# Kernel optimization log

Measured on AMD Instinct MI355X. Metric: run time of the kernel, lower is better.

## Reference

```python
import jax, jax.numpy as jnp
import numpy as np

D_MODEL = 1024
NUM_HEADS = 16
D_HEAD = D_MODEL // NUM_HEADS
PATCH = 128


def setup_inputs() -> dict:
    key = jax.random.key(0)
    ks = jax.random.split(key, 10)
    B, T = 4, 8192
    x = jax.random.normal(ks[0], (B, T, D_MODEL), dtype=jnp.float32)
    coords = jax.random.uniform(ks[1], (B, T, 2), dtype=jnp.float32)
    s = 1.0 / np.sqrt(D_MODEL)
    Wq = jax.random.normal(ks[2], (D_MODEL, D_MODEL), dtype=jnp.float32) * s
    Wk = jax.random.normal(ks[3], (D_MODEL, D_MODEL), dtype=jnp.float32) * s
    Wv = jax.random.normal(ks[4], (D_MODEL, D_MODEL), dtype=jnp.float32) * s
    Wo = jax.random.normal(ks[5], (D_MODEL, D_MODEL), dtype=jnp.float32) * s
    bq = jnp.zeros((D_MODEL,), jnp.float32)
    bk = jnp.zeros((D_MODEL,), jnp.float32)
    bv = jnp.zeros((D_MODEL,), jnp.float32)
    bo = jnp.zeros((D_MODEL,), jnp.float32)
    return {"x": x, "coords": coords, "Wq": Wq, "bq": bq, "Wk": Wk, "bk": bk,
            "Wv": Wv, "bv": bv, "Wo": Wo, "bo": bo}


def _patched_attn(x, Wq, bq, Wk, bk, Wv, bv, Wo, bo):
    B, T, D = x.shape
    P = PATCH
    pad_len = (P - T % P) % P
    if pad_len > 0:
        x = jnp.pad(x, ((0, 0), (0, pad_len), (0, 0)))
    Tp = T + pad_len
    n = Tp // P
    xp = x.reshape(B * n, P, D)  # [N, P, D], independent patches
    def heads(y):  # [N, P, D] -> [N, H, P, dh]
        return y.reshape(B * n, P, NUM_HEADS, D_HEAD).transpose(0, 2, 1, 3)
    q = heads(xp @ Wq + bq)
    k = heads(xp @ Wk + bk)
    v = heads(xp @ Wv + bv)
    scores = jnp.einsum('bhtd,bhTd->bhtT', q, k) / jnp.sqrt(jnp.asarray(D_HEAD, x.dtype))
    w = jax.nn.softmax(scores, axis=-1)
    out = jnp.einsum('bhtT,bhTd->bhtd', w, v)
    out = out.transpose(0, 2, 1, 3).reshape(B * n, P, D)
    out = out @ Wo + bo
    out = out.reshape(B, Tp, D)
    if pad_len > 0:
        out = out[:, :T, :]
    return out


def reference(x, coords, Wq, bq, Wk, bk, Wv, bv, Wo, bo):
    # coords participates only in padding/reshape, not in the math
    return _patched_attn(x, Wq, bq, Wk, bk, Wv, bv, Wo, bo)
```

## Files before the change

### kernel.cpp

```cpp
#include <hip/hip_runtime.h>
#include <hip/hip_bf16.h>


#define DEV static __device__ __forceinline__

typedef __attribute__((ext_vector_type(8))) short short8;
typedef __attribute__((ext_vector_type(4))) float f32x4;

DEV unsigned short f2b(float f) {
  unsigned u = __builtin_bit_cast(unsigned, f);
  u += 0x7fffu + ((u >> 16) & 1u);
  return (unsigned short)(u >> 16);
}

DEV void load_lds16(const void* g, void* l) {
  __builtin_amdgcn_global_load_lds(
      (const __attribute__((address_space(1))) void*)g,
      (__attribute__((address_space(3))) void*)l, 16, 0, 0);
}

#define MFMA_BF16(a, b, c) __builtin_amdgcn_mfma_f32_16x16x32_bf16((a), (b), (c), 0, 0, 0)
#define SB0() __builtin_amdgcn_sched_barrier(0)
#define BAR() __builtin_amdgcn_s_barrier()


__global__ void cvt_x_k(const float* __restrict__ x, unsigned short* __restrict__ xb, int n4) {
  int i = blockIdx.x * blockDim.x + threadIdx.x;
  int stride = gridDim.x * blockDim.x;
  for (; i < n4; i += stride) {
    float4 v = ((const float4*)x)[i];
    ushort4 o;
    o.x = f2b(v.x); o.y = f2b(v.y); o.z = f2b(v.z); o.w = f2b(v.w);
    ((ushort4*)xb)[i] = o;
  }
}

__global__ void twk4(const float* __restrict__ W0, const float* __restrict__ W1,
                     const float* __restrict__ W2, const float* __restrict__ W3,
                     unsigned short* __restrict__ Dqkv, unsigned short* __restrict__ Dot) {
  __shared__ unsigned short tile[64][65];
  const int w = blockIdx.x >> 8;
  const int t = blockIdx.x & 255;
  const float* W = (w == 0) ? W0 : (w == 1) ? W1 : (w == 2) ? W2 : W3;
  unsigned short* Wt = (w == 3) ? Dot : Dqkv + (size_t)w * 1024 * 1024;
  int k0 = (t >> 4) << 6;
  int n0 = (t & 15) << 6;
  int tx = threadIdx.x & 63;
  int ty = threadIdx.x >> 6;
#pragma unroll
  for (int i = 0; i < 16; ++i) {
    int r = (i << 2) + ty;
    tile[r][tx] = f2b(W[(size_t)(k0 + r) * 1024 + n0 + tx]);
  }
  __syncthreads();
#pragma unroll
  for (int i = 0; i < 16; ++i) {
    int n = (i << 2) + ty;
    Wt[(size_t)(n0 + n) * 1024 + k0 + tx] = tile[tx][n];
  }
}

__global__ void fuse_bias_k(const float* __restrict__ bq, const float* __restrict__ bk,
                            const float* __restrict__ bv, float* __restrict__ bqkv) {
  int i = blockIdx.x * 256 + threadIdx.x;
  if (i < 1024) bqkv[i] = bq[i];
  else if (i < 2048) bqkv[i] = bk[i - 1024];
  else if (i < 3072) bqkv[i] = bv[i - 2048];
}


template <bool OUT_F32>
__global__ __launch_bounds__(512, 2)
void gemm256(const unsigned short* __restrict__ A,
             const unsigned short* __restrict__ Bt,
             const float* __restrict__ bias,
             void* __restrict__ Cv, int M, int N, int K) {
  __shared__ __align__(16) unsigned short sh[65536];

  int nwg = gridDim.x, bid = blockIdx.x, wg = bid;
  if ((nwg & 7) == 0) {
    int cpx = nwg >> 3;
    wg = (bid & 7) * cpx + (bid >> 3);
  }
  const int nbn = N >> 8;
  const int bm = wg / nbn, bn = wg - bm * nbn;

  const int tid = threadIdx.x, lane = tid & 63, w = tid >> 6;
  const int wm = w >> 2, wn = w & 3;
  const int fr = lane & 15, g = lane >> 4;

  const int lr = lane >> 3;
  const int lb = ((lane & 7) << 4) ^ (lr << 4);
  const unsigned short* gsrc = (w < 4)
      ? A  + (size_t)(bm * 256 + w * 64 + lr) * K + (lb >> 1)
      : Bt + (size_t)(bn * 256 + (w - 4) * 64 + lr) * K + (lb >> 1);
  const int ldsw = w * 8192;

  const int koff0 = (g * 16) ^ ((fr & 7) << 4);
  const int koff1 = koff0 ^ 64;

  f32x4 acc[8][4] = {};
  const int NT = K >> 6;

  short8 a0[4][2], a1[4][2], b0[2][2], b1[2][2];

  {
    char* l0 = (char*)sh + ldsw;
    char* l1 = (char*)sh + 65536 + ldsw;
#pragma unroll
    for (int c = 0; c < 8; ++c)
      load_lds16(gsrc + (size_t)c * 8 * K, l0 + c * 1024);
#pragma unroll
    for (int c = 0; c < 8; ++c)
      load_lds16(gsrc + 64 + (size_t)c * 8 * K, l1 + c * 1024);
    asm volatile("s_waitcnt vmcnt(8)" ::: "memory");
    BAR();
    const char* ap = (const char*)sh + (wm * 128 + fr) * 128;
    const char* bp = (const char*)sh + 32768 + (wn * 64 + fr) * 128;
#pragma unroll
    for (int ii = 0; ii < 4; ++ii) {
      a0[ii][0] = *(const short8*)(ap + ii * 2048 + koff0);
      a0[ii][1] = *(const short8*)(ap + ii * 2048 + koff1);
    }
#pragma unroll
    for (int jj = 0; jj < 2; ++jj) {
      b0[jj][0] = *(const short8*)(bp + jj * 2048 + koff0);
      b0[jj][1] = *(const short8*)(bp + jj * 2048 + koff1);
    }
  }

  for (int t = 0; t < NT; ++t) {
    const char* bufc = (const char*)sh + (t & 1) * 65536;
    const char* bufn = (const char*)sh + ((t + 1) & 1) * 65536;
    const char* apc = bufc + (wm * 128 + fr) * 128;
    const char* bpc = bufc + 32768 + (wn * 64 + fr) * 128;

#pragma unroll
    for (int jj = 0; jj < 2; ++jj) {
      b1[jj][0] = *(const short8*)(bpc + 32 * 128 + jj * 2048 + koff0);
      b1[jj][1] = *(const short8*)(bpc + 32 * 128 + jj * 2048 + koff1);
    }
    BAR();
    asm volatile("s_waitcnt lgkmcnt(4)" ::: "memory");
    SB0();
    __builtin_amdgcn_s_setprio(1);
#pragma unroll
    for (int s = 0; s < 2; ++s)
#pragma unroll
      for (int ii = 0; ii < 4; ++ii)
#pragma unroll
        for (int jj = 0; jj < 2; ++jj)
          acc[ii][jj] = MFMA_BF16(a0[ii][s], b0[jj][s], acc[ii][jj]);
    __builtin_amdgcn_s_setprio(0);
    BAR();

#pragma unroll
    for (int ii = 0; ii < 4; ++ii) {
      a1[ii][0] = *(const short8*)(apc + 64 * 128 + ii * 2048 + koff0);
      a1[ii][1] = *(const short8*)(apc + 64 * 128 + ii * 2048 + koff1);
    }
    BAR();
    asm volatile("s_waitcnt lgkmcnt(8)" ::: "memory");
    SB0();
    __builtin_amdgcn_s_setprio(1);
#pragma unroll
    for (int s = 0; s < 2; ++s)
#pragma unroll
      for (int ii = 0; ii < 4; ++ii)
#pragma unroll
        for (int jj = 0; jj < 2; ++jj)
          acc[ii][2 + jj] = MFMA_BF16(a0[ii][s], b1[jj][s], acc[ii][2 + jj]);
    __builtin_amdgcn_s_setprio(0);
    SB0();
    asm volatile("s_waitcnt lgkmcnt(0)" ::: "memory");
    BAR();

    if (t + 2 < NT) {
      const unsigned short* sN = gsrc + (size_t)(t + 2) * 64;
      char* lN = (char*)sh + (t & 1) * 65536 + ldsw;
#pragma unroll
      for (int c = 0; c < 8; ++c)
        load_lds16(sN + (size_t)c * 8 * K, lN + c * 1024);
    }
    __builtin_amdgcn_s_setprio(1);
#pragma unroll
    for (int s = 0; s < 2; ++s)
#pragma unroll
      for (int ii = 0; ii < 4; ++ii)
#pragma unroll
        for (int jj = 0; jj < 2; ++jj)
          acc[4 + ii][2 + jj] = MFMA_BF16(a1[ii][s], b1[jj][s], acc[4 + ii][2 + jj]);
    __builtin_amdgcn_s_setprio(0);
    if (t + 2 < NT) {
      asm volatile("s_waitcnt vmcnt(8)" ::: "memory");
    } else {
      asm volatile("s_waitcnt vmcnt(0)" ::: "memory");
    }
    BAR();

    __builtin_amdgcn_s_setprio(1);
#pragma unroll
    for (int s = 0; s < 2; ++s)
#pragma unroll
      for (int ii = 0; ii < 4; ++ii)
#pragma unroll
        for (int jj = 0; jj < 2; ++jj)
          acc[4 + ii][jj] = MFMA_BF16(a1[ii][s], b0[jj][s], acc[4 + ii][jj]);
    __builtin_amdgcn_s_setprio(0);
    SB0();
    if (t + 1 < NT) {
      const char* apn = bufn + (wm * 128 + fr) * 128;
      const char* bpn = bufn + 32768 + (wn * 64 + fr) * 128;
#pragma unroll
      for (int ii = 0; ii < 4; ++ii) {
        a0[ii][0] = *(const short8*)(apn + ii * 2048 + koff0);
        a0[ii][1] = *(const short8*)(apn + ii * 2048 + koff1);
      }
#pragma unroll
      for (int jj = 0; jj < 2; ++jj) {
        b0[jj][0] = *(const short8*)(bpn + jj * 2048 + koff0);
        b0[jj][1] = *(const short8*)(bpn + jj * 2048 + koff1);
      }
    }
    SB0();
    BAR();
  }

  const int grow0 = bm * 256 + wm * 128 + g * 4;
  const int gcol0 = bn * 256 + wn * 64 + fr;
  float bv_[4];
#pragma unroll
  for (int j = 0; j < 4; ++j) bv_[j] = bias[gcol0 + j * 16];
#pragma unroll
  for (int i = 0; i < 8; ++i) {
    const int gr = grow0 + i * 16;
#pragma unroll
    for (int r = 0; r < 4; ++r) {
#pragma unroll
      for (int j = 0; j < 4; ++j) {
        float v = acc[i][j][r] + bv_[j];
        if (OUT_F32) ((float*)Cv)[(size_t)(gr + r) * N + gcol0 + j * 16] = v;
        else ((unsigned short*)Cv)[(size_t)(gr + r) * N + gcol0 + j * 16] = f2b(v);
      }
    }
  }
}


__global__ __launch_bounds__(256)
void attn_k(const unsigned short* __restrict__ qkv, unsigned short* __restrict__ out) {
  const int bh = blockIdx.x;
  const int p = bh >> 4, h = bh & 15;
  const int tid = threadIdx.x, lane = tid & 63, wv = tid >> 6;
  const int fr = lane & 15, fks = (lane >> 4) << 3;

  __shared__ __align__(16) unsigned short vt[64][136];
  __shared__ __align__(16) unsigned short pls[4][32][136];

  const size_t rowbase = (size_t)p * 128 * 3072;

  {
    const unsigned short* vsrc = qkv + rowbase + 2048 + (size_t)h * 64;
#pragma unroll
    for (int it = 0; it < 8; ++it) {
      int idx = tid + it * 256;
      int t = idx >> 4;
      int d4 = (idx & 15) << 2;
      ushort4 vv = *(const ushort4*)(vsrc + (size_t)t * 3072 + d4);
      vt[d4 + 0][t] = vv.x; vt[d4 + 1][t] = vv.y;
      vt[d4 + 2][t] = vv.z; vt[d4 + 3][t] = vv.w;
    }
  }

  short8 qf[2][2];
  {
    const unsigned short* qsrc = qkv + rowbase + (size_t)(wv * 32) * 3072 + h * 64;
#pragma unroll
    for (int mf = 0; mf < 2; ++mf)
#pragma unroll
      for (int kc = 0; kc < 2; ++kc)
        qf[mf][kc] = *(const short8*)(qsrc + (size_t)(mf * 16 + fr) * 3072 + kc * 32 + fks);
  }

  f32x4 s[2][8] = {};
  {
    const unsigned short* ksrc = qkv + rowbase + 1024 + (size_t)h * 64;
#pragma unroll
    for (int kc = 0; kc < 2; ++kc)
#pragma unroll
      for (int nf = 0; nf < 8; ++nf) {
        short8 kf = *(const short8*)(ksrc + (size_t)(nf * 16 + fr) * 3072 + kc * 32 + fks);
        s[0][nf] = MFMA_BF16(qf[0][kc], kf, s[0][nf]);
        s[1][nf] = MFMA_BF16(qf[1][kc], kf, s[1][nf]);
      }
  }
  __syncthreads();

  const float c0 = 0.125f * 1.44269504088896f;
  float sm[2][4];
#pragma unroll
  for (int mf = 0; mf < 2; ++mf)
#pragma unroll
    for (int r = 0; r < 4; ++r) {
      float m = s[mf][0][r];
#pragma unroll
      for (int nf = 1; nf < 8; ++nf) m = fmaxf(m, s[mf][nf][r]);
      m = fmaxf(m, __shfl_xor(m, 1));
      m = fmaxf(m, __shfl_xor(m, 2));
      m = fmaxf(m, __shfl_xor(m, 4));
      m = fmaxf(m, __shfl_xor(m, 8));
      float su = 0.f;
#pragma unroll
      for (int nf = 0; nf < 8; ++nf) {
        float e = exp2f((s[mf][nf][r] - m) * c0);
        s[mf][nf][r] = e;
        su += e;
      }
      su += __shfl_xor(su, 1);
      su += __shfl_xor(su, 2);
      su += __shfl_xor(su, 4);
      su += __shfl_xor(su, 8);
      sm[mf][r] = su;
    }

#pragma unroll
  for (int mf = 0; mf < 2; ++mf)
#pragma unroll
    for (int nf = 0; nf < 8; ++nf)
#pragma unroll
      for (int r = 0; r < 4; ++r)
        pls[wv][mf * 16 + ((lane >> 4) << 2) + r][nf * 16 + fr] = f2b(s[mf][nf][r]);

  f32x4 o[2][4] = {};
#pragma unroll
  for (int kc = 0; kc < 4; ++kc) {
    short8 pf0 = *(const short8*)&pls[wv][fr][kc * 32 + fks];
    short8 pf1 = *(const short8*)&pls[wv][16 + fr][kc * 32 + fks];
#pragma unroll
    for (int nf = 0; nf < 4; ++nf) {
      short8 vf = *(const short8*)&vt[nf * 16 + fr][kc * 32 + fks];
      o[0][nf] = MFMA_BF16(pf0, vf, o[0][nf]);
      o[1][nf] = MFMA_BF16(pf1, vf, o[1][nf]);
    }
  }

  unsigned short* obase = out + (size_t)(p * 128 + wv * 32) * 1024 + h * 64;
#pragma unroll
  for (int mf = 0; mf < 2; ++mf)
#pragma unroll
    for (int nf = 0; nf < 4; ++nf)
#pragma unroll
      for (int r = 0; r < 4; ++r) {
        int row = mf * 16 + ((lane >> 4) << 2) + r;
        float val = o[mf][nf][r] / sm[mf][r];
        obase[(size_t)row * 1024 + nf * 16 + fr] = f2b(val);
      }
}


extern "C" void kernel_launch(void* const* d_in, const int* in_sizes, int n_in,
                              void* d_out, int out_size, void* d_ws, size_t ws_size,
                              hipStream_t stream) {
  const float* x  = (const float*)d_in[0];
  const float* Wq = (const float*)d_in[2];
  const float* bq = (const float*)d_in[3];
  const float* Wk = (const float*)d_in[4];
  const float* bk = (const float*)d_in[5];
  const float* Wv = (const float*)d_in[6];
  const float* bv = (const float*)d_in[7];
  const float* Wo = (const float*)d_in[8];
  const float* bo = (const float*)d_in[9];

  char* ws = (char*)d_ws;
  unsigned short* xb   = (unsigned short*)(ws);
  unsigned short* wqkv = (unsigned short*)(ws + 67108864);
  unsigned short* wot  = (unsigned short*)(ws + 73400320);
  float*          bqkv = (float*)(ws + 75497472);
  unsigned short* qkv  = (unsigned short*)(ws + 75509760);

  cvt_x_k<<<2048, 256, 0, stream>>>(x, xb, (32768 * 1024) / 4);
  twk4<<<1024, 256, 0, stream>>>(Wq, Wk, Wv, Wo, wqkv, wot);
  fuse_bias_k<<<12, 256, 0, stream>>>(bq, bk, bv, bqkv);

  gemm256<false><<<1536, 512, 0, stream>>>(xb, wqkv, bqkv, qkv, 32768, 3072, 1024);
  attn_k<<<4096, 256, 0, stream>>>(qkv, xb);
  gemm256<true><<<512, 512, 0, stream>>>(xb, wot, bo, d_out, 32768, 1024, 1024);
}
```

Before: 631.1 us.

## Rewrite patch attention with 32x32 MFMA and register-resident probabilities

The attention kernel now uses 32x32x16 bf16 MFMAs and computes S transposed (K as the A operand), so each lane holds a full query row's scores. The row softmax therefore needs only a single cross-half shuffle. Probabilities are normalized and packed to bf16 with v_cvt_pk_bf16_f32, then rearranged with v_permlane32_swap directly into the A-operand layout, which removes the per-wave LDS staging buffer and its round trip. The V transpose into LDS now uses 4x4 register transposes with vector stores. This relies on MI355X-specific instructions and precise fragment-layout assumptions, and the final output stores remain scalar 2-byte writes.

```diff
diff --git a/kernel.cpp b/kernel.cpp
--- a/kernel.cpp
+++ b/kernel.cpp
@@ -6,6 +6,7 @@
 
 typedef __attribute__((ext_vector_type(8))) short short8;
 typedef __attribute__((ext_vector_type(4))) float f32x4;
+typedef __attribute__((ext_vector_type(16))) float f32x16;
 
 DEV unsigned short f2b(float f) {
   unsigned u = __builtin_bit_cast(unsigned, f);
@@ -13,6 +14,12 @@
   return (unsigned short)(u >> 16);
 }
 
+DEV unsigned cvtpk(float lo, float hi) {
+  unsigned r;
+  asm("v_cvt_pk_bf16_f32 %0, %1, %2" : "=v"(r) : "v"(lo), "v"(hi));
+  return r;
+}
+
 DEV void load_lds16(const void* g, void* l) {
   __builtin_amdgcn_global_load_lds(
       (const __attribute__((address_space(1))) void*)g,
@@ -20,6 +27,7 @@
 }
 
 #define MFMA_BF16(a, b, c) __builtin_amdgcn_mfma_f32_16x16x32_bf16((a), (b), (c), 0, 0, 0)
+#define MFMA32_BF16(a, b, c) __builtin_amdgcn_mfma_f32_32x32x16_bf16((a), (b), (c), 0, 0, 0)
 #define SB0() __builtin_amdgcn_sched_barrier(0)
 #define BAR() __builtin_amdgcn_s_barrier()
 
@@ -252,109 +260,106 @@
   const int bh = blockIdx.x;
   const int p = bh >> 4, h = bh & 15;
   const int tid = threadIdx.x, lane = tid & 63, wv = tid >> 6;
-  const int fr = lane & 15, fks = (lane >> 4) << 3;
+  const int c = lane & 31, hl = lane >> 5;
 
   __shared__ __align__(16) unsigned short vt[64][136];
-  __shared__ __align__(16) unsigned short pls[4][32][136];
 
   const size_t rowbase = (size_t)p * 128 * 3072;
 
   {
     const unsigned short* vsrc = qkv + rowbase + 2048 + (size_t)h * 64;
 #pragma unroll
-    for (int it = 0; it < 8; ++it) {
-      int idx = tid + it * 256;
-      int t = idx >> 4;
-      int d4 = (idx & 15) << 2;
-      ushort4 vv = *(const ushort4*)(vsrc + (size_t)t * 3072 + d4);
-      vt[d4 + 0][t] = vv.x; vt[d4 + 1][t] = vv.y;
-      vt[d4 + 2][t] = vv.z; vt[d4 + 3][t] = vv.w;
-    }
-  }
-
-  short8 qf[2][2];
+    for (int bb = 0; bb < 2; ++bb) {
+      int b = bb * 256 + tid;
+      int tg = b & 31, dg = b >> 5;
+      ushort4 ld[4];
+#pragma unroll
+      for (int i = 0; i < 4; ++i)
+        ld[i] = *(const ushort4*)(vsrc + (size_t)(tg * 4 + i) * 3072 + dg * 4);
+#pragma unroll
+      for (int j = 0; j < 4; ++j) {
+        ushort4 wr;
+        wr.x = ((const unsigned short*)&ld[0])[j];
+        wr.y = ((const unsigned short*)&ld[1])[j];
+        wr.z = ((const unsigned short*)&ld[2])[j];
+        wr.w = ((const unsigned short*)&ld[3])[j];
+        *(ushort4*)&vt[dg * 4 + j][tg * 4] = wr;
+      }
+    }
+  }
+
+  short8 qf[4];
   {
-    const unsigned short* qsrc = qkv + rowbase + (size_t)(wv * 32) * 3072 + h * 64;
-#pragma unroll
-    for (int mf = 0; mf < 2; ++mf)
-#pragma unroll
-      for (int kc = 0; kc < 2; ++kc)
-        qf[mf][kc] = *(const short8*)(qsrc + (size_t)(mf * 16 + fr) * 3072 + kc * 32 + fks);
-  }
-
-  f32x4 s[2][8] = {};
+    const unsigned short* qsrc = qkv + rowbase + (size_t)(wv * 32 + c) * 3072 + h * 64;
+#pragma unroll
+    for (int kc = 0; kc < 4; ++kc)
+      qf[kc] = *(const short8*)(qsrc + kc * 16 + hl * 8);
+  }
+
+  f32x16 st[4] = {};
   {
     const unsigned short* ksrc = qkv + rowbase + 1024 + (size_t)h * 64;
 #pragma unroll
-    for (int kc = 0; kc < 2; ++kc)
-#pragma unroll
-      for (int nf = 0; nf < 8; ++nf) {
-        short8 kf = *(const short8*)(ksrc + (size_t)(nf * 16 + fr) * 3072 + kc * 32 + fks);
-        s[0][nf] = MFMA_BF16(qf[0][kc], kf, s[0][nf]);
-        s[1][nf] = MFMA_BF16(qf[1][kc], kf, s[1][nf]);
-      }
-  }
+    for (int kf = 0; kf < 4; ++kf) {
+      const unsigned short* kr = ksrc + (size_t)(kf * 32 + c) * 3072 + hl * 8;
+      short8 kfr[4];
+#pragma unroll
+      for (int kc = 0; kc < 4; ++kc) kfr[kc] = *(const short8*)(kr + kc * 16);
+#pragma unroll
+      for (int kc = 0; kc < 4; ++kc)
+        st[kf] = MFMA32_BF16(kfr[kc], qf[kc], st[kf]);
+    }
+  }
+
+  const float c0 = 0.125f * 1.44269504088896f;
+  float m = st[0][0];
+#pragma unroll
+  for (int kf = 0; kf < 4; ++kf)
+#pragma unroll
+    for (int r = 0; r < 16; ++r) m = fmaxf(m, st[kf][r]);
+  m = fmaxf(m, __shfl_xor(m, 32));
+  float su = 0.f;
+#pragma unroll
+  for (int kf = 0; kf < 4; ++kf)
+#pragma unroll
+    for (int r = 0; r < 16; ++r) {
+      float e = exp2f((st[kf][r] - m) * c0);
+      st[kf][r] = e;
+      su += e;
+    }
+  su += __shfl_xor(su, 32);
+  const float inv = 1.0f / su;
+
   __syncthreads();
 
-  const float c0 = 0.125f * 1.44269504088896f;
-  float sm[2][4];
-#pragma unroll
-  for (int mf = 0; mf < 2; ++mf)
-#pragma unroll
-    for (int r = 0; r < 4; ++r) {
-      float m = s[mf][0][r];
-#pragma unroll
-      for (int nf = 1; nf < 8; ++nf) m = fmaxf(m, s[mf][nf][r]);
-      m = fmaxf(m, __shfl_xor(m, 1));
-      m = fmaxf(m, __shfl_xor(m, 2));
-      m = fmaxf(m, __shfl_xor(m, 4));
-      m = fmaxf(m, __shfl_xor(m, 8));
-      float su = 0.f;
-#pragma unroll
-      for (int nf = 0; nf < 8; ++nf) {
-        float e = exp2f((s[mf][nf][r] - m) * c0);
-        s[mf][nf][r] = e;
-        su += e;
-      }
-      su += __shfl_xor(su, 1);
-      su += __shfl_xor(su, 2);
-      su += __shfl_xor(su, 4);
-      su += __shfl_xor(su, 8);
-      sm[mf][r] = su;
-    }
-
-#pragma unroll
-  for (int mf = 0; mf < 2; ++mf)
-#pragma unroll
-    for (int nf = 0; nf < 8; ++nf)
-#pragma unroll
-      for (int r = 0; r < 4; ++r)
-        pls[wv][mf * 16 + ((lane >> 4) << 2) + r][nf * 16 + fr] = f2b(s[mf][nf][r]);
-
-  f32x4 o[2][4] = {};
-#pragma unroll
-  for (int kc = 0; kc < 4; ++kc) {
-    short8 pf0 = *(const short8*)&pls[wv][fr][kc * 32 + fks];
-    short8 pf1 = *(const short8*)&pls[wv][16 + fr][kc * 32 + fks];
-#pragma unroll
-    for (int nf = 0; nf < 4; ++nf) {
-      short8 vf = *(const short8*)&vt[nf * 16 + fr][kc * 32 + fks];
-      o[0][nf] = MFMA_BF16(pf0, vf, o[0][nf]);
-      o[1][nf] = MFMA_BF16(pf1, vf, o[1][nf]);
-    }
-  }
-
-  unsigned short* obase = out + (size_t)(p * 128 + wv * 32) * 1024 + h * 64;
-#pragma unroll
-  for (int mf = 0; mf < 2; ++mf)
-#pragma unroll
-    for (int nf = 0; nf < 4; ++nf)
-#pragma unroll
-      for (int r = 0; r < 4; ++r) {
-        int row = mf * 16 + ((lane >> 4) << 2) + r;
-        float val = o[mf][nf][r] / sm[mf][r];
-        obase[(size_t)row * 1024 + nf * 16 + fr] = f2b(val);
-      }
+  f32x16 ov[2] = {};
+#pragma unroll
+  for (int s = 0; s < 8; ++s) {
+    const int kf = s >> 1, a = (s & 1) * 8;
+    unsigned lo0 = cvtpk(st[kf][a + 0] * inv, st[kf][a + 1] * inv);
+    unsigned lo1 = cvtpk(st[kf][a + 2] * inv, st[kf][a + 3] * inv);
+    unsigned hi0 = cvtpk(st[kf][a + 4] * inv, st[kf][a + 5] * inv);
+    unsigned hi1 = cvtpk(st[kf][a + 6] * inv, st[kf][a + 7] * inv);
+    asm volatile("v_permlane32_swap_b32 %0, %1" : "+v"(lo0), "+v"(hi0));
+    asm volatile("v_permlane32_swap_b32 %0, %1" : "+v"(lo1), "+v"(hi1));
+    short8 pa;
+    ((unsigned*)&pa)[0] = lo0; ((unsigned*)&pa)[1] = lo1;
+    ((unsigned*)&pa)[2] = hi0; ((unsigned*)&pa)[3] = hi1;
+#pragma unroll
+    for (int df = 0; df < 2; ++df) {
+      short8 vf = *(const short8*)&vt[df * 32 + c][s * 16 + hl * 8];
+      ov[df] = MFMA32_BF16(pa, vf, ov[df]);
+    }
+  }
+
+  unsigned short* ob = out + (size_t)(p * 128 + wv * 32) * 1024 + h * 64;
+#pragma unroll
+  for (int df = 0; df < 2; ++df)
+#pragma unroll
+    for (int r = 0; r < 16; ++r) {
+      int q = (r & 3) + 8 * (r >> 2) + 4 * hl;
+      ob[(size_t)q * 1024 + df * 32 + c] = f2b(ov[df][r]);
+    }
 }
 
 
```

New measurement: 625.3 us. About the same (-0.9%).
